# Kernel optimization log

Hardware: AMD Instinct MI355X
Metric: run time of the kernel (lower is better)

The kernel has to match this reference:

```python
import jax, jax.numpy as jnp
import numpy as np

N_NODES = 50000
N_EDGES = 1600000
D_FEAT = 128
EPS = 1e-12  # matches F.normalize clamp_min eps


def setup_inputs() -> dict:
    key = jax.random.key(0)
    k1, k2 = jax.random.split(key)
    x = jax.random.normal(k1, (N_NODES, D_FEAT), dtype=jnp.float32)
    beta = jnp.ones((1,), dtype=jnp.float32)  # AGNNConv learnable scalar, init 1.0
    edge_index = jax.random.randint(k2, (2, N_EDGES), 0, N_NODES, dtype=jnp.int64)
    return {"x": x, "beta": beta, "edge_index": edge_index}


def reference(x, beta, edge_index):
    N = x.shape[0]
    # AGNNConv default add_self_loops=True
    loop = jnp.arange(N, dtype=edge_index.dtype)
    src = jnp.concatenate([edge_index[0], loop])  # j (source / message sender)
    dst = jnp.concatenate([edge_index[1], loop])  # i (target / aggregator)

    # cosine-similarity attention logits per edge, scaled by beta
    xn = x * jax.lax.rsqrt(jnp.maximum(jnp.sum(x * x, axis=-1, keepdims=True), EPS * EPS))
    logits = beta[0] * jnp.sum(xn[src] * xn[dst], axis=-1)  # [E+N]

    # segment softmax over incoming edges of each target node
    m = jax.ops.segment_max(logits, dst, num_segments=N)
    m = jax.lax.stop_gradient(m)
    e = jnp.exp(logits - m[dst])
    s = jax.ops.segment_sum(e, dst, num_segments=N)
    alpha = e / s[dst]  # self-loops guarantee s > 0

    # scatter-aggregate messages alpha_e * x_src
    out = jax.ops.segment_sum(alpha[:, None] * x[src], dst, num_segments=N)

    # wrapper: activation (relu); normalization=False; dropout p=0 -> identity
    return jax.nn.relu(out)
```

## Files before the change

### kernel.cpp

```cpp
#include <hip/hip_runtime.h>

#define NN 50000
#define NE 1600000
#define DF 128
#define NB 1250
#define BSZ 40
#define CAP 1664
#define NWGP 512
#define CHKP 3125
#define NBN 12500

static __device__ __forceinline__ float bflo(unsigned int u) {
    unsigned int v = u << 16; float f; __builtin_memcpy(&f, &v, 4); return f;
}
static __device__ __forceinline__ float bfhi(unsigned int u) {
    unsigned int v = u & 0xFFFF0000u; float f; __builtin_memcpy(&f, &v, 4); return f;
}
static __device__ __forceinline__ unsigned int f2bf(float f) {
    unsigned int u; __builtin_memcpy(&u, &f, 4);
    u += 0x7FFFu + ((u >> 16) & 1u);
    return u >> 16;
}

static __device__ __forceinline__ int block_excl_scan(int v, int t, int* wsum4) {
    int lane = t & 63, wv = t >> 6;
    int s = v;
    #pragma unroll
    for (int off = 1; off < 64; off <<= 1) {
        int u = __shfl_up(s, off);
        if (lane >= off) s += u;
    }
    if (lane == 63) wsum4[wv] = s;
    __syncthreads();
    int add = 0;
    #pragma unroll
    for (int w = 0; w < 4; ++w) add += (w < wv) ? wsum4[w] : 0;
    __syncthreads();
    return s + add - v;
}

__global__ __launch_bounds__(256)
void k_norm_part(const float* __restrict__ x,
                 const int* __restrict__ ei,
                 unsigned int* __restrict__ xn_bf,
                 float* __restrict__ norm,
                 int* __restrict__ cntG, int* __restrict__ offG,
                 unsigned int* __restrict__ pairs) {
    __shared__ int wsum4[4];
    __shared__ int cntL[NB];
    __shared__ int offL[NB];
    __shared__ unsigned int stg[CHKP];
    if (blockIdx.x >= NWGP) {
        int node = ((blockIdx.x - NWGP) * 256 + threadIdx.x) >> 6;
        int lane = threadIdx.x & 63;
        float2 v = ((const float2*)(x + (size_t)node * DF))[lane];
        float ss = v.x * v.x + v.y * v.y;
        #pragma unroll
        for (int m = 1; m < 64; m <<= 1) ss += __shfl_xor(ss, m);
        float rinv = rsqrtf(fmaxf(ss, 1e-24f));
        xn_bf[(size_t)node * 64 + lane] = (f2bf(v.y * rinv) << 16) | f2bf(v.x * rinv);
        if (lane == 0) norm[node] = ss * rinv;
        return;
    }
    int wg = blockIdx.x, t = threadIdx.x;
    const int* srcp = ei + wg * CHKP;
    const int* dstp = ei + NE + wg * CHKP;
    for (int i = t; i < NB; i += 256) cntL[i] = 0;
    __syncthreads();
    for (int i = t; i < CHKP; i += 256) atomicAdd(&cntL[dstp[i] / BSZ], 1);
    __syncthreads();
    {
        int base = t * 5;
        int loc[5];
        int s = 0;
        #pragma unroll
        for (int q = 0; q < 5; ++q) {
            int idx = base + q;
            int v = (idx < NB) ? cntL[idx] : 0;
            loc[q] = s;
            s += v;
        }
        int ex = block_excl_scan(s, t, wsum4);
        #pragma unroll
        for (int q = 0; q < 5; ++q) {
            int idx = base + q;
            if (idx < NB) offL[idx] = ex + loc[q];
        }
    }
    __syncthreads();
    for (int i = t; i < NB; i += 256) {
        cntG[wg * NB + i] = cntL[i];
        offG[wg * NB + i] = offL[i];
    }
    __syncthreads();
    for (int i = t; i < CHKP; i += 256) {
        int src = srcp[i];
        int dst = dstp[i];
        int b = dst / BSZ;
        int pos = atomicAdd(&offL[b], 1);
        stg[pos] = ((unsigned int)(dst - b * BSZ) << 16) | (unsigned int)src;
    }
    __syncthreads();
    unsigned int* chunk = pairs + (size_t)wg * CHKP;
    for (int i = t; i < CHKP; i += 256) chunk[i] = stg[i];
}

__global__ __launch_bounds__(256)
void k_build_gather(const unsigned int* __restrict__ xn_bf,
                    const float* __restrict__ norm,
                    const int* __restrict__ cntG, const int* __restrict__ offG,
                    const unsigned int* __restrict__ pairs,
                    const float* __restrict__ beta_p,
                    float* __restrict__ out) {
    __shared__ int wsum4[4];
    __shared__ unsigned int rawL[CAP];
    __shared__ unsigned int colL[CAP];
    __shared__ int hist[BSZ];
    __shared__ int rp[BSZ + 1];
    __shared__ int tot0, stotal;
    int b = blockIdx.x, t = threadIdx.x;

    int w0 = t, w1 = t + 256;
    int len0 = cntG[w0 * NB + b], off0 = offG[w0 * NB + b];
    int len1 = cntG[w1 * NB + b], off1 = offG[w1 * NB + b];
    int rb0 = block_excl_scan(len0, t, wsum4);
    if (t == 255) tot0 = rb0 + len0;
    int ex1 = block_excl_scan(len1, t, wsum4);
    int rb1 = tot0 + ex1;
    if (t == 255) stotal = rb1 + len1;
    __syncthreads();
    int cnt = stotal;
    if (cnt > CAP) cnt = CAP;
    {
        const unsigned int* s0 = pairs + (size_t)w0 * CHKP + off0;
        for (int q = 0; q < len0; ++q) {
            int pos = rb0 + q;
            if (pos < CAP) rawL[pos] = s0[q];
        }
        const unsigned int* s1 = pairs + (size_t)w1 * CHKP + off1;
        for (int q = 0; q < len1; ++q) {
            int pos = rb1 + q;
            if (pos < CAP) rawL[pos] = s1[q];
        }
    }
    if (t < BSZ) hist[t] = 0;
    __syncthreads();
    for (int i = t; i < cnt; i += 256) atomicAdd(&hist[rawL[i] >> 16], 1);
    __syncthreads();
    if (t < 64) {
        int v = (t < BSZ) ? hist[t] : 0;
        int s = v;
        #pragma unroll
        for (int off = 1; off < 64; off <<= 1) {
            int u = __shfl_up(s, off);
            if (t >= off) s += u;
        }
        if (t < BSZ) { rp[t + 1] = s; hist[t] = s - v; }
        if (t == 0) rp[0] = 0;
    }
    __syncthreads();
    for (int i = t; i < cnt; i += 256) {
        unsigned int p = rawL[i];
        unsigned int src = p & 0xFFFFu;
        int pos = atomicAdd(&hist[p >> 16], 1);
        colL[pos] = (f2bf(norm[src]) << 16) | src;
    }
    __syncthreads();

    int lane = t & 63;
    int w = t >> 6;
    int j = lane & 15;
    int g = lane >> 4;
    float beta = beta_p[0];
    float c = -fabsf(beta);
    for (int ln = w; ln < BSZ; ln += 4) {
        int node = b * BSZ + ln;
        uint4 du = ((const uint4*)(xn_bf + (size_t)node * 64))[j];
        float xd[8];
        #pragma unroll
        for (int q = 0; q < 4; ++q) {
            unsigned int u = (&du.x)[q];
            xd[2 * q]     = bflo(u);
            xd[2 * q + 1] = bfhi(u);
        }
        float acc[8] = {0.f, 0.f, 0.f, 0.f, 0.f, 0.f, 0.f, 0.f};
        float ssum = 0.f;
        int b0 = rp[ln], b1 = rp[ln + 1];

        int k = b0 + g;
        int kA = (k     < b1) ? k     : 0;
        int kB = (k + 4 < b1) ? k + 4 : 0;
        unsigned int pA = colL[kA];
        unsigned int pB = colL[kB];
        uint4 rA = ((const uint4*)(xn_bf + (size_t)(pA & 0xFFFFu) * 64))[j];
        uint4 rB = ((const uint4*)(xn_bf + (size_t)(pB & 0xFFFFu) * 64))[j];

        for (; k < b1; k += 8) {
            int kC = (k +  8 < b1) ? k +  8 : 0;
            int kD = (k + 12 < b1) ? k + 12 : 0;
            unsigned int pC = colL[kC];
            unsigned int pD = colL[kD];
            uint4 rC = ((const uint4*)(xn_bf + (size_t)(pC & 0xFFFFu) * 64))[j];
            uint4 rD = ((const uint4*)(xn_bf + (size_t)(pD & 0xFFFFu) * 64))[j];
            {
                float xs[8];
                #pragma unroll
                for (int q = 0; q < 4; ++q) {
                    unsigned int u = (&rA.x)[q];
                    xs[2 * q]     = bflo(u);
                    xs[2 * q + 1] = bfhi(u);
                }
                float dot = 0.f;
                #pragma unroll
                for (int q = 0; q < 8; ++q) dot = fmaf(xd[q], xs[q], dot);
                dot += __shfl_xor(dot, 1);
                dot += __shfl_xor(dot, 2);
                dot += __shfl_xor(dot, 4);
                dot += __shfl_xor(dot, 8);
                float e = __expf(fmaf(beta, dot, c));
                ssum += e;
                float wgt = e * bfhi(pA);
                #pragma unroll
                for (int q = 0; q < 8; ++q) acc[q] = fmaf(wgt, xs[q], acc[q]);
            }
            {
                float xs[8];
                #pragma unroll
                for (int q = 0; q < 4; ++q) {
                    unsigned int u = (&rB.x)[q];
                    xs[2 * q]     = bflo(u);
                    xs[2 * q + 1] = bfhi(u);
                }
                float dot = 0.f;
                #pragma unroll
                for (int q = 0; q < 8; ++q) dot = fmaf(xd[q], xs[q], dot);
                dot += __shfl_xor(dot, 1);
                dot += __shfl_xor(dot, 2);
                dot += __shfl_xor(dot, 4);
                dot += __shfl_xor(dot, 8);
                float e = __expf(fmaf(beta, dot, c));
                e = (k + 4 < b1) ? e : 0.f;
                ssum += e;
                float wgt = e * bfhi(pB);
                #pragma unroll
                for (int q = 0; q < 8; ++q) acc[q] = fmaf(wgt, xs[q], acc[q]);
            }
            pA = pC; pB = pD; rA = rC; rB = rD;
        }

        ssum += __shfl_xor(ssum, 16);
        ssum += __shfl_xor(ssum, 32);
        #pragma unroll
        for (int q = 0; q < 8; ++q) {
            acc[q] += __shfl_xor(acc[q], 16);
            acc[q] += __shfl_xor(acc[q], 32);
        }
        float e_self = __expf(beta + c);
        ssum += e_self;
        float wsl = e_self * norm[node];
        #pragma unroll
        for (int q = 0; q < 8; ++q) acc[q] = fmaf(wsl, xd[q], acc[q]);

        if (g == 0) {
            float inv = 1.0f / ssum;
            float4 o0, o1;
            o0.x = fmaxf(0.f, acc[0] * inv); o0.y = fmaxf(0.f, acc[1] * inv);
            o0.z = fmaxf(0.f, acc[2] * inv); o0.w = fmaxf(0.f, acc[3] * inv);
            o1.x = fmaxf(0.f, acc[4] * inv); o1.y = fmaxf(0.f, acc[5] * inv);
            o1.z = fmaxf(0.f, acc[6] * inv); o1.w = fmaxf(0.f, acc[7] * inv);
            float4* op = (float4*)(out + (size_t)node * DF + 8 * j);
            op[0] = o0;
            op[1] = o1;
        }
    }
}

extern "C" void kernel_launch(void* const* d_in, const int* in_sizes, int n_in,
                              void* d_out, int out_size, void* d_ws, size_t ws_size,
                              hipStream_t stream) {
    const float* x    = (const float*)d_in[0];
    const float* beta = (const float*)d_in[1];
    const int*   ei   = (const int*)d_in[2];
    float*       out  = (float*)d_out;

    char* ws = (char*)d_ws;
    unsigned int* xn_bf = (unsigned int*)ws;
    float* norm = (float*)(ws + 12800000);
    int*   cntG = (int*)  (ws + 13000000);
    int*   offG = (int*)  (ws + 15560000);
    unsigned int* pairs = (unsigned int*)(ws + 18120000);

    k_norm_part  <<<NWGP + NBN, 256, 0, stream>>>(x, ei, xn_bf, norm, cntG, offG, pairs);
    k_build_gather<<<NB,        256, 0, stream>>>(xn_bf, norm, cntG, offG, pairs, beta, out);
}
```

Baseline: 166.8 us.

## Split build and gather into separate kernels with packed descriptors and wide gather grid

Packs per-chunk count and offset into one 32-bit descriptor, halving descriptor traffic. The bucket build now copies raw pairs with 16 lanes per source chunk instead of one thread serially looping. The gather moves to its own kernel with one wave per node over a full-size grid, reading CSR columns from global memory, to raise occupancy and balance load. The cost is an extra launch and a global round trip for the column and row-pointer arrays.

```diff
diff --git a/kernel.cpp b/kernel.cpp
--- a/kernel.cpp
+++ b/kernel.cpp
@@ -44,7 +44,7 @@
                  const int* __restrict__ ei,
                  unsigned int* __restrict__ xn_bf,
                  float* __restrict__ norm,
-                 int* __restrict__ cntG, int* __restrict__ offG,
+                 unsigned int* __restrict__ descG,
                  unsigned int* __restrict__ pairs) {
     __shared__ int wsum4[4];
     __shared__ int cntL[NB];
@@ -88,10 +88,8 @@
         }
     }
     __syncthreads();
-    for (int i = t; i < NB; i += 256) {
-        cntG[wg * NB + i] = cntL[i];
-        offG[wg * NB + i] = offL[i];
-    }
+    for (int i = t; i < NB; i += 256)
+        descG[(size_t)wg * NB + i] = ((unsigned int)offL[i] << 16) | (unsigned int)cntL[i];
     __syncthreads();
     for (int i = t; i < CHKP; i += 256) {
         int src = srcp[i];
@@ -106,13 +104,13 @@
 }
 
 __global__ __launch_bounds__(256)
-void k_build_gather(const unsigned int* __restrict__ xn_bf,
-                    const float* __restrict__ norm,
-                    const int* __restrict__ cntG, const int* __restrict__ offG,
-                    const unsigned int* __restrict__ pairs,
-                    const float* __restrict__ beta_p,
-                    float* __restrict__ out) {
+void k_build(const float* __restrict__ norm,
+             const unsigned int* __restrict__ descG,
+             const unsigned int* __restrict__ pairs,
+             unsigned int* __restrict__ colG,
+             int2* __restrict__ rp2) {
     __shared__ int wsum4[4];
+    __shared__ int lenS[NWGP], offS[NWGP], rbase[NWGP];
     __shared__ unsigned int rawL[CAP];
     __shared__ unsigned int colL[CAP];
     __shared__ int hist[BSZ];
@@ -120,30 +118,32 @@
     __shared__ int tot0, stotal;
     int b = blockIdx.x, t = threadIdx.x;
 
-    int w0 = t, w1 = t + 256;
-    int len0 = cntG[w0 * NB + b], off0 = offG[w0 * NB + b];
-    int len1 = cntG[w1 * NB + b], off1 = offG[w1 * NB + b];
+    unsigned int d0 = descG[(size_t)t * NB + b];
+    unsigned int d1 = descG[(size_t)(t + 256) * NB + b];
+    int len0 = (int)(d0 & 0xFFFFu), off0 = (int)(d0 >> 16);
+    int len1 = (int)(d1 & 0xFFFFu), off1 = (int)(d1 >> 16);
     int rb0 = block_excl_scan(len0, t, wsum4);
     if (t == 255) tot0 = rb0 + len0;
     int ex1 = block_excl_scan(len1, t, wsum4);
     int rb1 = tot0 + ex1;
     if (t == 255) stotal = rb1 + len1;
+    lenS[t] = len0;        offS[t] = off0;        rbase[t] = rb0;
+    lenS[t + 256] = len1;  offS[t + 256] = off1;  rbase[t + 256] = rb1;
+    if (t < BSZ) hist[t] = 0;
     __syncthreads();
     int cnt = stotal;
     if (cnt > CAP) cnt = CAP;
-    {
-        const unsigned int* s0 = pairs + (size_t)w0 * CHKP + off0;
-        for (int q = 0; q < len0; ++q) {
-            int pos = rb0 + q;
-            if (pos < CAP) rawL[pos] = s0[q];
-        }
-        const unsigned int* s1 = pairs + (size_t)w1 * CHKP + off1;
-        for (int q = 0; q < len1; ++q) {
-            int pos = rb1 + q;
-            if (pos < CAP) rawL[pos] = s1[q];
-        }
-    }
-    if (t < BSZ) hist[t] = 0;
+
+    int g16 = t >> 4, l16 = t & 15;
+    for (int r = g16; r < NWGP; r += 16) {
+        int len = lenS[r];
+        int rb = rbase[r];
+        const unsigned int* sp = pairs + (size_t)r * CHKP + offS[r];
+        for (int q = l16; q < len; q += 16) {
+            int pos = rb + q;
+            if (pos < CAP) rawL[pos] = sp[q];
+        }
+    }
     __syncthreads();
     for (int i = t; i < cnt; i += 256) atomicAdd(&hist[rawL[i] >> 16], 1);
     __syncthreads();
@@ -166,112 +166,127 @@
         colL[pos] = (f2bf(norm[src]) << 16) | src;
     }
     __syncthreads();
-
-    int lane = t & 63;
-    int w = t >> 6;
+    int base = b * CAP;
+    for (int i = t; i < cnt; i += 256) colG[base + i] = colL[i];
+    if (t < BSZ) {
+        int2 v; v.x = base + rp[t]; v.y = base + rp[t + 1];
+        rp2[b * BSZ + t] = v;
+    }
+}
+
+__global__ __launch_bounds__(256)
+void k_gather(const unsigned int* __restrict__ xn_bf,
+              const float* __restrict__ norm,
+              const int2* __restrict__ rp2,
+              const unsigned int* __restrict__ colG,
+              const float* __restrict__ beta_p,
+              float* __restrict__ out) {
+    int node = (blockIdx.x * blockDim.x + threadIdx.x) >> 6;
+    int lane = threadIdx.x & 63;
+    if (node >= NN) return;
     int j = lane & 15;
     int g = lane >> 4;
     float beta = beta_p[0];
     float c = -fabsf(beta);
-    for (int ln = w; ln < BSZ; ln += 4) {
-        int node = b * BSZ + ln;
-        uint4 du = ((const uint4*)(xn_bf + (size_t)node * 64))[j];
-        float xd[8];
-        #pragma unroll
-        for (int q = 0; q < 4; ++q) {
-            unsigned int u = (&du.x)[q];
-            xd[2 * q]     = bflo(u);
-            xd[2 * q + 1] = bfhi(u);
-        }
-        float acc[8] = {0.f, 0.f, 0.f, 0.f, 0.f, 0.f, 0.f, 0.f};
-        float ssum = 0.f;
-        int b0 = rp[ln], b1 = rp[ln + 1];
-
-        int k = b0 + g;
-        int kA = (k     < b1) ? k     : 0;
-        int kB = (k + 4 < b1) ? k + 4 : 0;
-        unsigned int pA = colL[kA];
-        unsigned int pB = colL[kB];
-        uint4 rA = ((const uint4*)(xn_bf + (size_t)(pA & 0xFFFFu) * 64))[j];
-        uint4 rB = ((const uint4*)(xn_bf + (size_t)(pB & 0xFFFFu) * 64))[j];
-
-        for (; k < b1; k += 8) {
-            int kC = (k +  8 < b1) ? k +  8 : 0;
-            int kD = (k + 12 < b1) ? k + 12 : 0;
-            unsigned int pC = colL[kC];
-            unsigned int pD = colL[kD];
-            uint4 rC = ((const uint4*)(xn_bf + (size_t)(pC & 0xFFFFu) * 64))[j];
-            uint4 rD = ((const uint4*)(xn_bf + (size_t)(pD & 0xFFFFu) * 64))[j];
-            {
-                float xs[8];
-                #pragma unroll
-                for (int q = 0; q < 4; ++q) {
-                    unsigned int u = (&rA.x)[q];
-                    xs[2 * q]     = bflo(u);
-                    xs[2 * q + 1] = bfhi(u);
-                }
-                float dot = 0.f;
-                #pragma unroll
-                for (int q = 0; q < 8; ++q) dot = fmaf(xd[q], xs[q], dot);
-                dot += __shfl_xor(dot, 1);
-                dot += __shfl_xor(dot, 2);
-                dot += __shfl_xor(dot, 4);
-                dot += __shfl_xor(dot, 8);
-                float e = __expf(fmaf(beta, dot, c));
-                ssum += e;
-                float wgt = e * bfhi(pA);
-                #pragma unroll
-                for (int q = 0; q < 8; ++q) acc[q] = fmaf(wgt, xs[q], acc[q]);
+
+    uint4 du = ((const uint4*)(xn_bf + (size_t)node * 64))[j];
+    float xd[8];
+    #pragma unroll
+    for (int q = 0; q < 4; ++q) {
+        unsigned int u = (&du.x)[q];
+        xd[2 * q]     = bflo(u);
+        xd[2 * q + 1] = bfhi(u);
+    }
+
+    float acc[8] = {0.f, 0.f, 0.f, 0.f, 0.f, 0.f, 0.f, 0.f};
+    float ssum = 0.f;
+    int2 rr = rp2[node];
+    int b0 = rr.x, b1 = rr.y;
+
+    int k = b0 + g;
+    int kA = (k     < b1) ? k     : 0;
+    int kB = (k + 4 < b1) ? k + 4 : 0;
+    unsigned int pA = colG[kA];
+    unsigned int pB = colG[kB];
+    uint4 rA = ((const uint4*)(xn_bf + (size_t)(pA & 0xFFFFu) * 64))[j];
+    uint4 rB = ((const uint4*)(xn_bf + (size_t)(pB & 0xFFFFu) * 64))[j];
+
+    for (; k < b1; k += 8) {
+        int kC = (k +  8 < b1) ? k +  8 : 0;
+        int kD = (k + 12 < b1) ? k + 12 : 0;
+        unsigned int pC = colG[kC];
+        unsigned int pD = colG[kD];
+        uint4 rC = ((const uint4*)(xn_bf + (size_t)(pC & 0xFFFFu) * 64))[j];
+        uint4 rD = ((const uint4*)(xn_bf + (size_t)(pD & 0xFFFFu) * 64))[j];
+        {
+            float xs[8];
+            #pragma unroll
+            for (int q = 0; q < 4; ++q) {
+                unsigned int u = (&rA.x)[q];
+                xs[2 * q]     = bflo(u);
+                xs[2 * q + 1] = bfhi(u);
             }
-            {
-                float xs[8];
-                #pragma unroll
-                for (int q = 0; q < 4; ++q) {
-                    unsigned int u = (&rB.x)[q];
-                    xs[2 * q]     = bflo(u);
-                    xs[2 * q + 1] = bfhi(u);
-                }
-                float dot = 0.f;
-                #pragma unroll
-                for (int q = 0; q < 8; ++q) dot = fmaf(xd[q], xs[q], dot);
-                dot += __shfl_xor(dot, 1);
-                dot += __shfl_xor(dot, 2);
-                dot += __shfl_xor(dot, 4);
-                dot += __shfl_xor(dot, 8);
-                float e = __expf(fmaf(beta, dot, c));
-                e = (k + 4 < b1) ? e : 0.f;
-                ssum += e;
-                float wgt = e * bfhi(pB);
-                #pragma unroll
-                for (int q = 0; q < 8; ++q) acc[q] = fmaf(wgt, xs[q], acc[q]);
+            float dot = 0.f;
+            #pragma unroll
+            for (int q = 0; q < 8; ++q) dot = fmaf(xd[q], xs[q], dot);
+            dot += __shfl_xor(dot, 1);
+            dot += __shfl_xor(dot, 2);
+            dot += __shfl_xor(dot, 4);
+            dot += __shfl_xor(dot, 8);
+            float e = __expf(fmaf(beta, dot, c));
+            ssum += e;
+            float wgt = e * bfhi(pA);
+            #pragma unroll
+            for (int q = 0; q < 8; ++q) acc[q] = fmaf(wgt, xs[q], acc[q]);
+        }
+        {
+            float xs[8];
+            #pragma unroll
+            for (int q = 0; q < 4; ++q) {
+                unsigned int u = (&rB.x)[q];
+                xs[2 * q]     = bflo(u);
+                xs[2 * q + 1] = bfhi(u);
             }
-            pA = pC; pB = pD; rA = rC; rB = rD;
-        }
-
-        ssum += __shfl_xor(ssum, 16);
-        ssum += __shfl_xor(ssum, 32);
-        #pragma unroll
-        for (int q = 0; q < 8; ++q) {
-            acc[q] += __shfl_xor(acc[q], 16);
-            acc[q] += __shfl_xor(acc[q], 32);
-        }
-        float e_self = __expf(beta + c);
-        ssum += e_self;
-        float wsl = e_self * norm[node];
-        #pragma unroll
-        for (int q = 0; q < 8; ++q) acc[q] = fmaf(wsl, xd[q], acc[q]);
-
-        if (g == 0) {
-            float inv = 1.0f / ssum;
-            float4 o0, o1;
-            o0.x = fmaxf(0.f, acc[0] * inv); o0.y = fmaxf(0.f, acc[1] * inv);
-            o0.z = fmaxf(0.f, acc[2] * inv); o0.w = fmaxf(0.f, acc[3] * inv);
-            o1.x = fmaxf(0.f, acc[4] * inv); o1.y = fmaxf(0.f, acc[5] * inv);
-            o1.z = fmaxf(0.f, acc[6] * inv); o1.w = fmaxf(0.f, acc[7] * inv);
-            float4* op = (float4*)(out + (size_t)node * DF + 8 * j);
-            op[0] = o0;
-            op[1] = o1;
-        }
+            float dot = 0.f;
+            #pragma unroll
+            for (int q = 0; q < 8; ++q) dot = fmaf(xd[q], xs[q], dot);
+            dot += __shfl_xor(dot, 1);
+            dot += __shfl_xor(dot, 2);
+            dot += __shfl_xor(dot, 4);
+            dot += __shfl_xor(dot, 8);
+            float e = __expf(fmaf(beta, dot, c));
+            e = (k + 4 < b1) ? e : 0.f;
+            ssum += e;
+            float wgt = e * bfhi(pB);
+            #pragma unroll
+            for (int q = 0; q < 8; ++q) acc[q] = fmaf(wgt, xs[q], acc[q]);
+        }
+        pA = pC; pB = pD; rA = rC; rB = rD;
+    }
+
+    ssum += __shfl_xor(ssum, 16);
+    ssum += __shfl_xor(ssum, 32);
+    #pragma unroll
+    for (int q = 0; q < 8; ++q) {
+        acc[q] += __shfl_xor(acc[q], 16);
+        acc[q] += __shfl_xor(acc[q], 32);
+    }
+    float e_self = __expf(beta + c);
+    ssum += e_self;
+    float wsl = e_self * norm[node];
+    #pragma unroll
+    for (int q = 0; q < 8; ++q) acc[q] = fmaf(wsl, xd[q], acc[q]);
+
+    if (g == 0) {
+        float inv = 1.0f / ssum;
+        float4 o0, o1;
+        o0.x = fmaxf(0.f, acc[0] * inv); o0.y = fmaxf(0.f, acc[1] * inv);
+        o0.z = fmaxf(0.f, acc[2] * inv); o0.w = fmaxf(0.f, acc[3] * inv);
+        o1.x = fmaxf(0.f, acc[4] * inv); o1.y = fmaxf(0.f, acc[5] * inv);
+        o1.z = fmaxf(0.f, acc[6] * inv); o1.w = fmaxf(0.f, acc[7] * inv);
+        float4* op = (float4*)(out + (size_t)node * DF + 8 * j);
+        op[0] = o0;
+        op[1] = o1;
     }
 }
 
@@ -286,10 +301,12 @@
     char* ws = (char*)d_ws;
     unsigned int* xn_bf = (unsigned int*)ws;
     float* norm = (float*)(ws + 12800000);
-    int*   cntG = (int*)  (ws + 13000000);
-    int*   offG = (int*)  (ws + 15560000);
-    unsigned int* pairs = (unsigned int*)(ws + 18120000);
-
-    k_norm_part  <<<NWGP + NBN, 256, 0, stream>>>(x, ei, xn_bf, norm, cntG, offG, pairs);
-    k_build_gather<<<NB,        256, 0, stream>>>(xn_bf, norm, cntG, offG, pairs, beta, out);
-}
+    unsigned int* descG = (unsigned int*)(ws + 13000000);
+    unsigned int* pairs = (unsigned int*)(ws + 15560000);
+    unsigned int* colG  = (unsigned int*)(ws + 21960000);
+    int2* rp2 = (int2*)(ws + 30280000);
+
+    k_norm_part<<<NWGP + NBN, 256, 0, stream>>>(x, ei, xn_bf, norm, descG, pairs);
+    k_build    <<<NB,         256, 0, stream>>>(norm, descG, pairs, colG, rp2);
+    k_gather   <<<(NN * 64 + 255) / 256, 256, 0, stream>>>(xn_bf, norm, rp2, colG, beta, out);
+}
```

Measured after the change: 167.0 us. Within noise of the previous version (+0.2%).
